# Kernel optimization log

Hardware: AMD Instinct MI355X
Metric: run time of the kernel (lower is better)

Reference implementation:

```python
import jax, jax.numpy as jnp
import numpy as np

BN_EPS = 1e-5


def _gin_layer(x, src, dst, Wa, ba, Wb, bb, n_nodes):
    # GINConv (eps=0): h_i = MLP(x_i + sum_{j in N(i)} x_j)
    agg = jax.ops.segment_sum(x[src], dst, num_segments=n_nodes)
    h = x + agg
    h = jnp.maximum(h @ Wa + ba, 0.0) @ Wb + bb
    return h


def _bn(x, g, b, m, v):
    return (x - m) * jax.lax.rsqrt(v + BN_EPS) * g + b


def setup_inputs() -> dict:
    key = jax.random.key(0)
    ks = jax.random.split(key, 32)
    N, F, D, C, E = 50000, 128, 32, 10, 800000
    inp = {
        "x": jax.random.normal(ks[0], (N, F), dtype=jnp.float32),
        "edge_index": jax.random.randint(ks[1], (2, E), 0, N, dtype=jnp.int32),
    }
    def lin(k, fi, fo):
        s = 1.0 / np.sqrt(fi)
        kw, kb = jax.random.split(k)
        return (jax.random.uniform(kw, (fi, fo), jnp.float32, -s, s),
                jax.random.uniform(kb, (fo,), jnp.float32, -s, s))
    inp["W1a"], inp["b1a"] = lin(ks[2], F, D)
    inp["W1b"], inp["b1b"] = lin(ks[3], D, D)
    inp["W2a"], inp["b2a"] = lin(ks[4], D, D)
    inp["W2b"], inp["b2b"] = lin(ks[5], D, D)
    inp["W3a"], inp["b3a"] = lin(ks[6], D, D)
    inp["W3b"], inp["b3b"] = lin(ks[7], D, D)
    for i in (1, 2, 3):
        inp[f"g{i}"] = jnp.ones((D,), jnp.float32)
        inp[f"be{i}"] = jnp.zeros((D,), jnp.float32)
        inp[f"m{i}"] = jax.random.normal(ks[8 + i], (D,), jnp.float32) * 0.1
        inp[f"v{i}"] = jax.random.uniform(ks[12 + i], (D,), jnp.float32, 0.5, 1.5)
    inp["Wf1"], inp["bf1"] = lin(ks[20], D, D)
    inp["Wf2"], inp["bf2"] = lin(ks[21], D, C)
    return inp


def reference(x, edge_index,
              W1a, b1a, W1b, b1b, W2a, b2a, W2b, b2b, W3a, b3a, W3b, b3b,
              g1, be1, m1, v1, g2, be2, m2, v2, g3, be3, m3, v3,
              Wf1, bf1, Wf2, bf2):
    n = x.shape[0]
    src, dst = edge_index[0], edge_index[1]
    h = jnp.maximum(_gin_layer(x, src, dst, W1a, b1a, W1b, b1b, n), 0.0)
    h = _bn(h, g1, be1, m1, v1)
    h = jnp.maximum(_gin_layer(h, src, dst, W2a, b2a, W2b, b2b, n), 0.0)
    h = _bn(h, g2, be2, m2, v2)
    h = jnp.maximum(_gin_layer(h, src, dst, W3a, b3a, W3b, b3b, n), 0.0)
    h = _bn(h, g3, be3, m3, v3)
    h = jnp.maximum(h @ Wf1 + bf1, 0.0)
    # dropout is identity in inference mode
    h = h @ Wf2 + bf2
    return jax.nn.log_softmax(h, axis=-1)
```

## Files before the change

kernel.cpp:

```cpp
#include <hip/hip_runtime.h>

#define BN_EPS 1e-5f
#define PART_STRIPES 160
#define CAP 64

__global__ void zero_ints(int* __restrict__ p, int n4) {
    int i = blockIdx.x * blockDim.x + threadIdx.x;
    if (i < n4) reinterpret_cast<int4*>(p)[i] = make_int4(0, 0, 0, 0);
}

__global__ void gemm128to32(const float* __restrict__ x, const float* __restrict__ W,
                            float* __restrict__ z, int n) {
    __shared__ __align__(16) float sW[128 * 32];
    __shared__ __align__(16) float sIn[32][132];
    int tid = threadIdx.x;
    for (int i = tid; i < 128 * 32; i += 256)
        sW[i] = W[i];
    {
        int base = blockIdx.x * 32;
        #pragma unroll
        for (int q = 0; q < 4; q++) {
            int flat = tid * 4 + q * 1024;
            int r = flat >> 7, cc = flat & 127;
            int node = base + r;
            float4 xv = make_float4(0.f, 0.f, 0.f, 0.f);
            if (node < n) xv = *reinterpret_cast<const float4*>(x + (size_t)node * 128 + cc);
            *reinterpret_cast<float4*>(&sIn[r][cc]) = xv;
        }
    }
    __syncthreads();

    int grp = tid >> 3, lane = tid & 7, c = lane * 4;
    int node = blockIdx.x * 32 + grp;
    float4 acc = make_float4(0.f, 0.f, 0.f, 0.f);
    #pragma unroll 8
    for (int k4 = 0; k4 < 32; k4++) {
        const float4 t4 = *reinterpret_cast<const float4*>(&sIn[grp][k4 * 4]);
        #pragma unroll
        for (int kk = 0; kk < 4; kk++) {
            float tk = (kk == 0) ? t4.x : (kk == 1) ? t4.y : (kk == 2) ? t4.z : t4.w;
            const float4 w = *reinterpret_cast<const float4*>(&sW[(k4 * 4 + kk) * 32 + c]);
            acc.x += tk * w.x; acc.y += tk * w.y; acc.z += tk * w.z; acc.w += tk * w.w;
        }
    }
    if (node < n) *reinterpret_cast<float4*>(z + (size_t)node * 32 + c) = acc;
}

__global__ void place_edges_fixed(const int* __restrict__ src, const int* __restrict__ dst,
                                  int* __restrict__ cursor, int* __restrict__ ssrc,
                                  int E, int n) {
    int g = blockIdx.x & 7;
    int sb = blockIdx.x >> 3;
    int rstep = (n + 7) / 8;
    int lo = g * rstep;
    int hi = lo + rstep; if (hi > n) hi = n;
    int per = (E + PART_STRIPES - 1) / PART_STRIPES;
    int e0 = sb * per;
    int e1 = e0 + per; if (e1 > E) e1 = E;
    for (int e = e0 + threadIdx.x; e < e1; e += blockDim.x) {
        int d = dst[e];
        if (d >= lo && d < hi) {
            int k = atomicAdd(&cursor[d], 1);
            if (k < CAP) ssrc[((size_t)d << 6) + k] = src[e];
        }
    }
}

#define GATHER_BODY(zptr)                                                        \
    int j = j0;                                                                  \
    for (; j + 7 < j1; j += 8) {                                                 \
        int idxv = ssrc[j + lane];                                               \
        int s0 = __shfl(idxv, 0, 8); int s1 = __shfl(idxv, 1, 8);                \
        int s2 = __shfl(idxv, 2, 8); int s3 = __shfl(idxv, 3, 8);                \
        int s4 = __shfl(idxv, 4, 8); int s5 = __shfl(idxv, 5, 8);                \
        int s6 = __shfl(idxv, 6, 8); int s7 = __shfl(idxv, 7, 8);                \
        float4 v0 = *reinterpret_cast<const float4*>(zptr + (size_t)s0 * 32 + c);\
        float4 v1 = *reinterpret_cast<const float4*>(zptr + (size_t)s1 * 32 + c);\
        float4 v2 = *reinterpret_cast<const float4*>(zptr + (size_t)s2 * 32 + c);\
        float4 v3 = *reinterpret_cast<const float4*>(zptr + (size_t)s3 * 32 + c);\
        float4 v4 = *reinterpret_cast<const float4*>(zptr + (size_t)s4 * 32 + c);\
        float4 v5 = *reinterpret_cast<const float4*>(zptr + (size_t)s5 * 32 + c);\
        float4 v6 = *reinterpret_cast<const float4*>(zptr + (size_t)s6 * 32 + c);\
        float4 v7 = *reinterpret_cast<const float4*>(zptr + (size_t)s7 * 32 + c);\
        acc.x += (v0.x + v1.x) + (v2.x + v3.x);                                  \
        acc.y += (v0.y + v1.y) + (v2.y + v3.y);                                  \
        acc.z += (v0.z + v1.z) + (v2.z + v3.z);                                  \
        acc.w += (v0.w + v1.w) + (v2.w + v3.w);                                  \
        acc2.x += (v4.x + v5.x) + (v6.x + v7.x);                                 \
        acc2.y += (v4.y + v5.y) + (v6.y + v7.y);                                 \
        acc2.z += (v4.z + v5.z) + (v6.z + v7.z);                                 \
        acc2.w += (v4.w + v5.w) + (v6.w + v7.w);                                 \
    }                                                                            \
    for (; j + 1 < j1; j += 2) {                                                 \
        int s0 = ssrc[j];     int s1 = ssrc[j + 1];                              \
        float4 v0 = *reinterpret_cast<const float4*>(zptr + (size_t)s0 * 32 + c);\
        float4 v1 = *reinterpret_cast<const float4*>(zptr + (size_t)s1 * 32 + c);\
        acc.x += v0.x + v1.x; acc.y += v0.y + v1.y;                              \
        acc.z += v0.z + v1.z; acc.w += v0.w + v1.w;                              \
    }                                                                            \
    if (j < j1) {                                                                \
        int s0 = ssrc[j];                                                        \
        float4 v0 = *reinterpret_cast<const float4*>(zptr + (size_t)s0 * 32 + c);\
        acc.x += v0.x; acc.y += v0.y; acc.z += v0.z; acc.w += v0.w;              \
    }                                                                            \
    acc.x += acc2.x; acc.y += acc2.y; acc.z += acc2.z; acc.w += acc2.w;

#define MATMUL32(sWx, hv)                                                        \
    _Pragma("unroll")                                                            \
    for (int k4 = 0; k4 < 8; k4++) {                                             \
        const float4 t4 = *reinterpret_cast<const float4*>(&sT[grp][k4 * 4]);    \
        const float4 wa = *reinterpret_cast<const float4*>(&sWx[(k4 * 4 + 0) * 32 + c]); \
        const float4 wb = *reinterpret_cast<const float4*>(&sWx[(k4 * 4 + 1) * 32 + c]); \
        const float4 wc = *reinterpret_cast<const float4*>(&sWx[(k4 * 4 + 2) * 32 + c]); \
        const float4 wd = *reinterpret_cast<const float4*>(&sWx[(k4 * 4 + 3) * 32 + c]); \
        hv.x += t4.x * wa.x + t4.y * wb.x + t4.z * wc.x + t4.w * wd.x;           \
        hv.y += t4.x * wa.y + t4.y * wb.y + t4.z * wc.y + t4.w * wd.y;           \
        hv.z += t4.x * wa.z + t4.y * wb.z + t4.z * wc.z + t4.w * wd.z;           \
        hv.w += t4.x * wa.w + t4.y * wb.w + t4.z * wc.w + t4.w * wd.w;           \
    }

__global__ void gin_fused_mid(const float* __restrict__ z, const int* __restrict__ cnt,
                              const int* __restrict__ ssrc,
                              const float* __restrict__ ba, const float* __restrict__ Wb,
                              const float* __restrict__ bb,
                              const float* __restrict__ g, const float* __restrict__ be,
                              const float* __restrict__ m, const float* __restrict__ v,
                              const float* __restrict__ Wn, float* __restrict__ zout, int n) {
    __shared__ __align__(16) float sWb[1024];
    __shared__ __align__(16) float sWn[1024];
    __shared__ __align__(16) float sT[32][36];
    int tid = threadIdx.x;
    for (int i = tid; i < 1024; i += 256) { sWb[i] = Wb[i]; sWn[i] = Wn[i]; }
    int grp = tid >> 3, lane = tid & 7, c = lane * 4;
    int node = blockIdx.x * 32 + grp;

    float4 acc = make_float4(0.f, 0.f, 0.f, 0.f);
    float4 acc2 = make_float4(0.f, 0.f, 0.f, 0.f);
    int j0 = 0, j1 = 0;
    if (node < n) {
        acc = *reinterpret_cast<const float4*>(z + (size_t)node * 32 + c);
        int d = cnt[node]; d = d < CAP ? d : CAP;
        j0 = node << 6;
        j1 = j0 + d;
    }
    GATHER_BODY(z)

    const float4 bav = *reinterpret_cast<const float4*>(ba + c);
    sT[grp][c + 0] = fmaxf(acc.x + bav.x, 0.0f);
    sT[grp][c + 1] = fmaxf(acc.y + bav.y, 0.0f);
    sT[grp][c + 2] = fmaxf(acc.z + bav.z, 0.0f);
    sT[grp][c + 3] = fmaxf(acc.w + bav.w, 0.0f);
    __syncthreads();

    float4 h = *reinterpret_cast<const float4*>(bb + c);
    MATMUL32(sWb, h)
    const float4 mv = *reinterpret_cast<const float4*>(m + c);
    const float4 vv = *reinterpret_cast<const float4*>(v + c);
    const float4 gv = *reinterpret_cast<const float4*>(g + c);
    const float4 bev = *reinterpret_cast<const float4*>(be + c);
    float4 o;
    o.x = (fmaxf(h.x, 0.f) - mv.x) * rsqrtf(vv.x + BN_EPS) * gv.x + bev.x;
    o.y = (fmaxf(h.y, 0.f) - mv.y) * rsqrtf(vv.y + BN_EPS) * gv.y + bev.y;
    o.z = (fmaxf(h.z, 0.f) - mv.z) * rsqrtf(vv.z + BN_EPS) * gv.z + bev.z;
    o.w = (fmaxf(h.w, 0.f) - mv.w) * rsqrtf(vv.w + BN_EPS) * gv.w + bev.w;
    __syncthreads();
    sT[grp][c + 0] = o.x;
    sT[grp][c + 1] = o.y;
    sT[grp][c + 2] = o.z;
    sT[grp][c + 3] = o.w;
    __syncthreads();

    float4 zq = make_float4(0.f, 0.f, 0.f, 0.f);
    MATMUL32(sWn, zq)
    if (node < n) *reinterpret_cast<float4*>(zout + (size_t)node * 32 + c) = zq;
}

__global__ void gin_fused_last(const float* __restrict__ z, const int* __restrict__ cnt,
                               const int* __restrict__ ssrc,
                               const float* __restrict__ ba, const float* __restrict__ Wb,
                               const float* __restrict__ bb,
                               const float* __restrict__ g, const float* __restrict__ be,
                               const float* __restrict__ m, const float* __restrict__ v,
                               const float* __restrict__ Wf1, const float* __restrict__ bf1,
                               const float* __restrict__ Wf2, const float* __restrict__ bf2,
                               float* __restrict__ out, int n) {
    __shared__ __align__(16) float sWb[1024];
    __shared__ __align__(16) float sW1[1024];
    __shared__ float sW2[320];
    __shared__ __align__(16) float sT[32][36];
    __shared__ float sZ[32][12];
    int tid = threadIdx.x;
    for (int i = tid; i < 1024; i += 256) { sWb[i] = Wb[i]; sW1[i] = Wf1[i]; }
    for (int i = tid; i < 320; i += 256) sW2[i] = Wf2[i];
    int grp = tid >> 3, lane = tid & 7, c = lane * 4;
    int node = blockIdx.x * 32 + grp;

    float4 acc = make_float4(0.f, 0.f, 0.f, 0.f);
    float4 acc2 = make_float4(0.f, 0.f, 0.f, 0.f);
    int j0 = 0, j1 = 0;
    if (node < n) {
        acc = *reinterpret_cast<const float4*>(z + (size_t)node * 32 + c);
        int d = cnt[node]; d = d < CAP ? d : CAP;
        j0 = node << 6;
        j1 = j0 + d;
    }
    GATHER_BODY(z)

    const float4 bav = *reinterpret_cast<const float4*>(ba + c);
    sT[grp][c + 0] = fmaxf(acc.x + bav.x, 0.0f);
    sT[grp][c + 1] = fmaxf(acc.y + bav.y, 0.0f);
    sT[grp][c + 2] = fmaxf(acc.z + bav.z, 0.0f);
    sT[grp][c + 3] = fmaxf(acc.w + bav.w, 0.0f);
    __syncthreads();

    float4 h = *reinterpret_cast<const float4*>(bb + c);
    MATMUL32(sWb, h)
    const float4 mv = *reinterpret_cast<const float4*>(m + c);
    const float4 vv = *reinterpret_cast<const float4*>(v + c);
    const float4 gv = *reinterpret_cast<const float4*>(g + c);
    const float4 bev = *reinterpret_cast<const float4*>(be + c);
    float4 o;
    o.x = (fmaxf(h.x, 0.f) - mv.x) * rsqrtf(vv.x + BN_EPS) * gv.x + bev.x;
    o.y = (fmaxf(h.y, 0.f) - mv.y) * rsqrtf(vv.y + BN_EPS) * gv.y + bev.y;
    o.z = (fmaxf(h.z, 0.f) - mv.z) * rsqrtf(vv.z + BN_EPS) * gv.z + bev.z;
    o.w = (fmaxf(h.w, 0.f) - mv.w) * rsqrtf(vv.w + BN_EPS) * gv.w + bev.w;
    __syncthreads();
    sT[grp][c + 0] = o.x;
    sT[grp][c + 1] = o.y;
    sT[grp][c + 2] = o.z;
    sT[grp][c + 3] = o.w;
    __syncthreads();

    float4 t2 = *reinterpret_cast<const float4*>(bf1 + c);
    MATMUL32(sW1, t2)
    t2.x = fmaxf(t2.x, 0.f); t2.y = fmaxf(t2.y, 0.f);
    t2.z = fmaxf(t2.z, 0.f); t2.w = fmaxf(t2.w, 0.f);
    __syncthreads();
    sT[grp][c + 0] = t2.x;
    sT[grp][c + 1] = t2.y;
    sT[grp][c + 2] = t2.z;
    sT[grp][c + 3] = t2.w;
    __syncthreads();

    for (int jj = lane; jj < 10; jj += 8) {
        float l = bf2[jj];
        #pragma unroll
        for (int k4 = 0; k4 < 8; k4++) {
            const float4 t4 = *reinterpret_cast<const float4*>(&sT[grp][k4 * 4]);
            l += t4.x * sW2[(k4 * 4 + 0) * 10 + jj];
            l += t4.y * sW2[(k4 * 4 + 1) * 10 + jj];
            l += t4.z * sW2[(k4 * 4 + 2) * 10 + jj];
            l += t4.w * sW2[(k4 * 4 + 3) * 10 + jj];
        }
        sZ[grp][jj] = l;
    }
    __syncthreads();

    if (node < n) {
        float mx = sZ[grp][0];
        #pragma unroll
        for (int jj = 1; jj < 10; jj++) mx = fmaxf(mx, sZ[grp][jj]);
        float s = 0.0f;
        #pragma unroll
        for (int jj = 0; jj < 10; jj++) s += __expf(sZ[grp][jj] - mx);
        float lse = mx + logf(s);
        for (int jj = lane; jj < 10; jj += 8)
            out[(size_t)node * 10 + jj] = sZ[grp][jj] - lse;
    }
}

extern "C" void kernel_launch(void* const* d_in, const int* in_sizes, int n_in,
                              void* d_out, int out_size, void* d_ws, size_t ws_size,
                              hipStream_t stream) {
    const float* x   = (const float*)d_in[0];
    const int*   ei  = (const int*)d_in[1];
    const float* W1a = (const float*)d_in[2];
    const float* b1a = (const float*)d_in[3];
    const float* W1b = (const float*)d_in[4];
    const float* b1b = (const float*)d_in[5];
    const float* W2a = (const float*)d_in[6];
    const float* b2a = (const float*)d_in[7];
    const float* W2b = (const float*)d_in[8];
    const float* b2b = (const float*)d_in[9];
    const float* W3a = (const float*)d_in[10];
    const float* b3a = (const float*)d_in[11];
    const float* W3b = (const float*)d_in[12];
    const float* b3b = (const float*)d_in[13];
    const float* g1  = (const float*)d_in[14];
    const float* be1 = (const float*)d_in[15];
    const float* m1  = (const float*)d_in[16];
    const float* v1  = (const float*)d_in[17];
    const float* g2  = (const float*)d_in[18];
    const float* be2 = (const float*)d_in[19];
    const float* m2  = (const float*)d_in[20];
    const float* v2  = (const float*)d_in[21];
    const float* g3  = (const float*)d_in[22];
    const float* be3 = (const float*)d_in[23];
    const float* m3  = (const float*)d_in[24];
    const float* v3  = (const float*)d_in[25];
    const float* Wf1 = (const float*)d_in[26];
    const float* bf1 = (const float*)d_in[27];
    const float* Wf2 = (const float*)d_in[28];
    const float* bf2 = (const float*)d_in[29];

    const int n = in_sizes[0] / 128;
    const int E = in_sizes[1] / 2;
    const int* src = ei;
    const int* dst = ei + E;

    float* zA = (float*)d_ws;
    float* zB = zA + (size_t)n * 32;
    int* cursor = (int*)(zB + (size_t)n * 32);
    int* ssrc   = cursor + n;

    float* out = (float*)d_out;
    const int nodeBlocks32 = (n + 31) / 32;
    const int nz4 = (n + 3) / 4;

    zero_ints<<<(nz4 + 255) / 256, 256, 0, stream>>>(cursor, nz4);
    place_edges_fixed<<<PART_STRIPES * 8, 256, 0, stream>>>(src, dst, cursor, ssrc, E, n);

    gemm128to32<<<nodeBlocks32, 256, 0, stream>>>(x, W1a, zA, n);
    gin_fused_mid<<<nodeBlocks32, 256, 0, stream>>>(zA, cursor, ssrc, b1a, W1b, b1b,
                                                    g1, be1, m1, v1, W2a, zB, n);
    gin_fused_mid<<<nodeBlocks32, 256, 0, stream>>>(zB, cursor, ssrc, b2a, W2b, b2b,
                                                    g2, be2, m2, v2, W3a, zA, n);
    gin_fused_last<<<nodeBlocks32, 256, 0, stream>>>(zA, cursor, ssrc, b3a, W3b, b3b,
                                                     g3, be3, m3, v3, Wf1, bf1, Wf2, bf2,
                                                     out, n);
}
```

Before: 125.7 us.

## Merge edge placement and first-layer GEMM into one launch with vectorized edge reads

```diff
diff --git a/kernel.cpp b/kernel.cpp
--- a/kernel.cpp
+++ b/kernel.cpp
@@ -9,15 +9,52 @@
     if (i < n4) reinterpret_cast<int4*>(p)[i] = make_int4(0, 0, 0, 0);
 }
 
-__global__ void gemm128to32(const float* __restrict__ x, const float* __restrict__ W,
-                            float* __restrict__ z, int n) {
+__global__ void place_and_gemm(const int* __restrict__ src, const int* __restrict__ dst,
+                               int* __restrict__ cursor, int* __restrict__ ssrc,
+                               int E, int n,
+                               const float* __restrict__ x, const float* __restrict__ W,
+                               float* __restrict__ z, int placeBlocks) {
     __shared__ __align__(16) float sW[128 * 32];
     __shared__ __align__(16) float sIn[32][132];
+    int b = blockIdx.x;
+    if (b < placeBlocks) {
+        int g = b & 7;
+        int sb = b >> 3;
+        int rstep = (n + 7) / 8;
+        int lo = g * rstep;
+        int hi = lo + rstep; if (hi > n) hi = n;
+        int per = (E + PART_STRIPES - 1) / PART_STRIPES;
+        int e0 = sb * per;
+        int e1 = e0 + per; if (e1 > E) e1 = E;
+
+        auto doedge = [&](int d, int s) {
+            if (d >= lo && d < hi) {
+                int k = atomicAdd(&cursor[d], 1);
+                if (k < CAP) ssrc[((size_t)d << 6) + k] = s;
+            }
+        };
+        for (int base = e0 + threadIdx.x * 4; base < e1; base += 1024) {
+            if (base + 3 < e1) {
+                const int4 d4 = *reinterpret_cast<const int4*>(dst + base);
+                const int4 s4 = *reinterpret_cast<const int4*>(src + base);
+                doedge(d4.x, s4.x);
+                doedge(d4.y, s4.y);
+                doedge(d4.z, s4.z);
+                doedge(d4.w, s4.w);
+            } else {
+                int stop = base + 4; if (stop > e1) stop = e1;
+                for (int e = base; e < stop; e++) doedge(dst[e], src[e]);
+            }
+        }
+        return;
+    }
+
+    int blk = b - placeBlocks;
     int tid = threadIdx.x;
     for (int i = tid; i < 128 * 32; i += 256)
         sW[i] = W[i];
     {
-        int base = blockIdx.x * 32;
+        int base = blk * 32;
         #pragma unroll
         for (int q = 0; q < 4; q++) {
             int flat = tid * 4 + q * 1024;
@@ -31,7 +68,7 @@
     __syncthreads();
 
     int grp = tid >> 3, lane = tid & 7, c = lane * 4;
-    int node = blockIdx.x * 32 + grp;
+    int node = blk * 32 + grp;
     float4 acc = make_float4(0.f, 0.f, 0.f, 0.f);
     #pragma unroll 8
     for (int k4 = 0; k4 < 32; k4++) {
@@ -44,26 +81,6 @@
         }
     }
     if (node < n) *reinterpret_cast<float4*>(z + (size_t)node * 32 + c) = acc;
-}
-
-__global__ void place_edges_fixed(const int* __restrict__ src, const int* __restrict__ dst,
-                                  int* __restrict__ cursor, int* __restrict__ ssrc,
-                                  int E, int n) {
-    int g = blockIdx.x & 7;
-    int sb = blockIdx.x >> 3;
-    int rstep = (n + 7) / 8;
-    int lo = g * rstep;
-    int hi = lo + rstep; if (hi > n) hi = n;
-    int per = (E + PART_STRIPES - 1) / PART_STRIPES;
-    int e0 = sb * per;
-    int e1 = e0 + per; if (e1 > E) e1 = E;
-    for (int e = e0 + threadIdx.x; e < e1; e += blockDim.x) {
-        int d = dst[e];
-        if (d >= lo && d < hi) {
-            int k = atomicAdd(&cursor[d], 1);
-            if (k < CAP) ssrc[((size_t)d << 6) + k] = src[e];
-        }
-    }
 }
 
 #define GATHER_BODY(zptr)                                                        \
@@ -315,12 +332,13 @@
 
     float* out = (float*)d_out;
     const int nodeBlocks32 = (n + 31) / 32;
+    const int placeBlocks = PART_STRIPES * 8;
     const int nz4 = (n + 3) / 4;
 
     zero_ints<<<(nz4 + 255) / 256, 256, 0, stream>>>(cursor, nz4);
-    place_edges_fixed<<<PART_STRIPES * 8, 256, 0, stream>>>(src, dst, cursor, ssrc, E, n);
-
-    gemm128to32<<<nodeBlocks32, 256, 0, stream>>>(x, W1a, zA, n);
+    place_and_gemm<<<placeBlocks + nodeBlocks32, 256, 0, stream>>>(
+        src, dst, cursor, ssrc, E, n, x, W1a, zA, placeBlocks);
+
     gin_fused_mid<<<nodeBlocks32, 256, 0, stream>>>(zA, cursor, ssrc, b1a, W1b, b1b,
                                                     g1, be1, m1, v1, W2a, zB, n);
     gin_fused_mid<<<nodeBlocks32, 256, 0, stream>>>(zB, cursor, ssrc, b2a, W2b, b2b,
```

Measured after the change: 117.8 us. 1.07x faster.
